# Kernel tuning notes

Hardware: AMD Instinct MI355X
Metric: run time of the kernel (lower is better)

Reference implementation:

```python
import jax, jax.numpy as jnp
import numpy as np

EPS = 1e-5

def _bn(x, gamma, beta):
    # BatchNorm1d training-mode math: batch mean / biased variance over edge dim
    mean = jnp.mean(x, axis=0)
    var = jnp.mean(jnp.square(x - mean), axis=0)
    return (x - mean) * (gamma / jnp.sqrt(var + EPS)) + beta


def setup_inputs() -> dict:
    key = jax.random.key(0)
    ks = jax.random.split(key, 12)
    n, d, s, h, e = 50000, 256, 32, 128, 500000
    feat = 3 * d + s + 1  # 801
    sc = lambda fan_in: 1.0 / np.sqrt(fan_in)
    return {
        "node_embeddings": jax.random.normal(ks[0], (n, d), jnp.float32),
        "gradient_scores": jax.random.normal(ks[1], (e,), jnp.float32),
        "step_embedding": jax.random.normal(ks[2], (s,), jnp.float32),
        "W1": jax.random.normal(ks[3], (feat, h), jnp.float32) * sc(feat),
        "b1": jnp.zeros((h,), jnp.float32),
        "g1": jnp.ones((h,), jnp.float32),
        "be1": jnp.zeros((h,), jnp.float32),
        "W2": jax.random.normal(ks[4], (h, h // 2), jnp.float32) * sc(h),
        "b2": jnp.zeros((h // 2,), jnp.float32),
        "g2": jnp.ones((h // 2,), jnp.float32),
        "be2": jnp.zeros((h // 2,), jnp.float32),
        "W3": jax.random.normal(ks[5], (h // 2, 1), jnp.float32) * sc(h // 2),
        "b3": jnp.zeros((1,), jnp.float32),
        "edge_index": jax.random.randint(ks[6], (2, e), 0, n, jnp.int64),
    }


def reference(node_embeddings, gradient_scores, step_embedding,
              W1, b1, g1, be1, W2, b2, g2, be2, W3, b3, edge_index):
    src, dst = edge_index[0], edge_index[1]
    h_u = node_embeddings[src]              # [E, d]
    h_v = node_embeddings[dst]              # [E, d]
    edge_diff = jnp.abs(h_u - h_v)          # [E, d]
    E = edge_index.shape[1]
    step = jnp.broadcast_to(step_embedding[None, :], (E, step_embedding.shape[0]))
    feats = jnp.concatenate([h_u, h_v, edge_diff, step, gradient_scores[:, None]], axis=1)
    x = jnp.maximum(feats @ W1 + b1, 0.0)
    x = _bn(x, g1, be1)                     # dropout is identity in eval
    x = jnp.maximum(x @ W2 + b2, 0.0)
    x = _bn(x, g2, be2)
    out = jnp.tanh(x @ W3 + b3)[:, 0]       # [E]
    return out
```

## Files before the change

kernel.cpp:

```cpp
#include <hip/hip_runtime.h>

#define NE 500000
#define DIMK 256
#define H1 128
#define H2 64
#define EPSBN 1e-5f
#define GRID1 512
#define NT1 1954
#define GRID2 512
#define NJOBS2 NT1

typedef _Float16 half8 __attribute__((ext_vector_type(8)));
typedef float f32x4 __attribute__((ext_vector_type(4)));
typedef unsigned short ushort8 __attribute__((ext_vector_type(8)));

typedef const __attribute__((address_space(1))) void* gas1_t;
typedef __attribute__((address_space(3))) void* las3_t;

static __device__ __forceinline__ half8 habs8(half8 x) {
  ushort8 u = __builtin_bit_cast(ushort8, x);
  u &= (unsigned short)0x7FFF;
  return __builtin_bit_cast(half8, u);
}
static __device__ __forceinline__ float h2f(unsigned int u) {
  return (float)__builtin_bit_cast(_Float16, (unsigned short)(u & 0xffff));
}
static __device__ __forceinline__ unsigned packf16(float a, float b) {
  unsigned lo = (unsigned)__builtin_bit_cast(unsigned short, (_Float16)a);
  unsigned hi = (unsigned)__builtin_bit_cast(unsigned short, (_Float16)b);
  return lo | (hi << 16);
}
static __device__ __forceinline__ void gload_lds16(const _Float16* src, _Float16* dst) {
  __builtin_amdgcn_global_load_lds((gas1_t)src, (las3_t)dst, 16, 0, 0);
}

#define SB0 __builtin_amdgcn_sched_barrier(0)

__global__ void k_preall(const float* __restrict__ emb, _Float16* __restrict__ embh,
                         const float* __restrict__ W1, _Float16* __restrict__ bfrag,
                         const float* __restrict__ b1, const float* __restrict__ step,
                         float* __restrict__ c0) {
  const int bid = blockIdx.x, t = threadIdx.x;
  if (bid < 6250) {
    const int i = (bid * 256 + t) * 8;
    const float4 a = *(const float4*)(emb + i);
    const float4 b = *(const float4*)(emb + i + 4);
    half8 h;
    h[0] = (_Float16)a.x; h[1] = (_Float16)a.y; h[2] = (_Float16)a.z; h[3] = (_Float16)a.w;
    h[4] = (_Float16)b.x; h[5] = (_Float16)b.y; h[6] = (_Float16)b.z; h[7] = (_Float16)b.w;
    *(half8*)(embh + i) = h;
  } else if (bid < 6298) {
    const int g = (bid - 6250) * 256 + t;
    const int lane = g & 63, f = g >> 6;
    const int c = f & 7, kc = (f >> 3) & 7, s = f >> 6;
    const int row0 = s * 256 + kc * 32 + (lane >> 4) * 8;
    const int col = c * 16 + (lane & 15);
    half8 h;
#pragma unroll
    for (int j = 0; j < 8; ++j) h[j] = (_Float16)W1[(row0 + j) * H1 + col];
    *(half8*)(bfrag + (size_t)g * 8) = h;
  } else {
    if (t < H1) {
      float a = b1[t];
#pragma unroll
      for (int tt = 0; tt < 32; ++tt) a += step[tt] * W1[(768 + tt) * H1 + t];
      c0[t] = a;
    }
  }
}

#define STAGE1(q, kcv) do {                                                   \
    _Pragma("unroll")                                                         \
    for (int jj = 0; jj < 6; ++jj) {                                          \
      const int sc = jj * 4 + w;                                              \
      const int ff = (sc >> 3) * 64 + (kcv) * 8 + (sc & 7);                   \
      gload_lds16(bfrag + ((size_t)ff * 64 + lane) * 8,                       \
                  s_B + (size_t)(q) * 12288 + sc * 512);                      \
    }                                                                         \
  } while (0)

__global__ __launch_bounds__(256, 2)
void k_layer1(const _Float16* __restrict__ embh, const void* __restrict__ eidx_raw,
              const float* __restrict__ grad, const float* __restrict__ W1,
              const float* __restrict__ c0, const _Float16* __restrict__ bfrag,
              _Float16* __restrict__ x1, float* __restrict__ p1) {
  __shared__ int s_src[256], s_dst[256];
  __shared__ float s_g[256];
  __shared__ float s_wg[128], s_c0[128], s_sum[128], s_sq[128];
  __shared__ __align__(16) _Float16 s_B[2 * 12288];

  const int t = threadIdx.x, bid = blockIdx.x;
  const int w = t >> 6, lane = t & 63, quad = lane >> 4, m15 = lane & 15;

  if (t < 128) {
    s_wg[t] = W1[800 * H1 + t];
    s_c0[t] = c0[t];
    s_sum[t] = 0.f; s_sq[t] = 0.f;
  }

  const unsigned* ew = (const unsigned*)eidx_raw;
  const bool is64 = ((ew[1] | ew[3] | ew[5] | ew[7]) == 0u);
  const int* e32 = (const int*)eidx_raw;
  const long long* e64 = (const long long*)eidx_raw;

  float st_s[8] = {0, 0, 0, 0, 0, 0, 0, 0}, st_q[8] = {0, 0, 0, 0, 0, 0, 0, 0};

  for (int tile = bid; tile < NT1; tile += GRID1) {
    const int base = tile * 256;
    __syncthreads();
    {
      int e = base + t; if (e >= NE) e = NE - 1;
      if (is64) { s_src[t] = (int)e64[e]; s_dst[t] = (int)e64[NE + e]; }
      else      { s_src[t] = e32[e];      s_dst[t] = e32[NE + e]; }
      s_g[t] = grad[e];
    }
    STAGE1(0, 0);
    __syncthreads();

    const int r0 = w * 64 + m15;
    const _Float16* pu[4];
    const _Float16* pv[4];
#pragma unroll
    for (int r = 0; r < 4; ++r) {
      pu[r] = embh + (size_t)s_src[r0 + r * 16] * DIMK + quad * 8;
      pv[r] = embh + (size_t)s_dst[r0 + r * 16] * DIMK + quad * 8;
    }
    f32x4 acc[4][8];
#pragma unroll
    for (int r = 0; r < 4; ++r)
#pragma unroll
      for (int c = 0; c < 8; ++c) acc[r][c] = (f32x4)0.f;

#pragma unroll 1
    for (int kc = 0; kc < 8; ++kc) {
      half8 u[4], v[4];
#pragma unroll
      for (int r = 0; r < 4; ++r) {
        u[r] = *(const half8*)(pu[r] + kc * 32);
        v[r] = *(const half8*)(pv[r] + kc * 32);
      }
      SB0;
      asm volatile("s_waitcnt vmcnt(8)" ::: "memory");
      __builtin_amdgcn_s_barrier();
      SB0;
      if (kc < 7) STAGE1((kc + 1) & 1, kc + 1);
      SB0;
      half8 d[4];
#pragma unroll
      for (int r = 0; r < 4; ++r) d[r] = habs8(u[r] - v[r]);

      const half8* bq = (const half8*)s_B + (size_t)(kc & 1) * 1536 + lane;
#pragma unroll
      for (int c = 0; c < 8; ++c) {
        const half8 bu = bq[c * 64];
        const half8 bv = bq[512 + c * 64];
        const half8 bd = bq[1024 + c * 64];
#pragma unroll
        for (int r = 0; r < 4; ++r)
          acc[r][c] = __builtin_amdgcn_mfma_f32_16x16x32_f16(u[r], bu, acc[r][c], 0, 0, 0);
#pragma unroll
        for (int r = 0; r < 4; ++r)
          acc[r][c] = __builtin_amdgcn_mfma_f32_16x16x32_f16(v[r], bv, acc[r][c], 0, 0, 0);
#pragma unroll
        for (int r = 0; r < 4; ++r)
          acc[r][c] = __builtin_amdgcn_mfma_f32_16x16x32_f16(d[r], bd, acc[r][c], 0, 0, 0);
      }
      SB0;
    }
#pragma unroll
    for (int r = 0; r < 4; ++r) {
      const int erow = w * 64 + r * 16 + quad * 4;
#pragma unroll
      for (int c = 0; c < 8; ++c) {
        const int colL = c * 16 + m15;
        const float wgv = s_wg[colL], c0v = s_c0[colL];
#pragma unroll
        for (int reg = 0; reg < 4; ++reg) {
          const int e = base + erow + reg;
          float x = acc[r][c][reg] + s_g[erow + reg] * wgv + c0v;
          x = fmaxf(x, 0.f);
          if (e >= NE) x = 0.f;
          st_s[c] += x; st_q[c] += x * x;
          if (e < NE) x1[(size_t)e * H1 + colL] = (_Float16)x;
        }
      }
    }
  }
  __syncthreads();
#pragma unroll
  for (int c = 0; c < 8; ++c) {
    float a = st_s[c]; a += __shfl_xor(a, 16); a += __shfl_xor(a, 32);
    float b = st_q[c]; b += __shfl_xor(b, 16); b += __shfl_xor(b, 32);
    if (lane < 16) { atomicAdd(&s_sum[c * 16 + m15], a); atomicAdd(&s_sq[c * 16 + m15], b); }
  }
  __syncthreads();
  if (t < 128) {
    p1[t * GRID1 + bid] = s_sum[t];
    p1[128 * GRID1 + t * GRID1 + bid] = s_sq[t];
  }
}

__global__ void k_fin1(const float* __restrict__ p1, const float* __restrict__ g1,
                       const float* __restrict__ be1, const float* __restrict__ W2,
                       const float* __restrict__ b2, float* __restrict__ w2f,
                       float* __restrict__ b2f) {
  __shared__ float s1[128], t1[128];
  const int t = threadIdx.x;
  if (t < 128) {
    float s = 0.f, q = 0.f;
    const float4* rs = (const float4*)(p1 + t * GRID1);
    const float4* rq = (const float4*)(p1 + 128 * GRID1 + t * GRID1);
#pragma unroll 4
    for (int i = 0; i < GRID1 / 4; ++i) {
      float4 a = rs[i]; s += a.x + a.y + a.z + a.w;
      float4 b = rq[i]; q += b.x + b.y + b.z + b.w;
    }
    const float inv = 1.0f / (float)NE;
    float mean = s * inv;
    float var = q * inv - mean * mean;
    float sc = g1[t] * rsqrtf(var + EPSBN);
    s1[t] = sc; t1[t] = be1[t] - mean * sc;
  }
  __syncthreads();
  for (int i = t; i < H1 * H2; i += 256) w2f[i] = s1[i >> 6] * W2[i];
  if (t < 64) {
    float b = b2[t];
    for (int j = 0; j < 128; ++j) b += t1[j] * W2[j * 64 + t];
    b2f[t] = b;
  }
}

__global__ __launch_bounds__(256, 2)
void k_layer2(const _Float16* __restrict__ x1, const float* __restrict__ w2f,
              const float* __restrict__ b2f, _Float16* __restrict__ x2,
              float* __restrict__ p2) {
  __shared__ __align__(16) _Float16 b_lds[8192];
  __shared__ float s_b[64], s_sum[64], s_sq[64];
  const int t = threadIdx.x, bid = blockIdx.x;
  const int w = t >> 6, lane = t & 63, quad = lane >> 4, m15 = lane & 15;

  for (int i = t; i < 8192; i += 256) {
    const int j = i & 7, li = (i >> 3) & 63, f = i >> 9;
    const int c = f & 3, kk = f >> 2;
    const int row = kk * 32 + (li >> 4) * 8 + j;
    const int col = c * 16 + (li & 15);
    b_lds[i] = (_Float16)w2f[row * H2 + col];
  }
  if (t < 64) { s_b[t] = b2f[t]; s_sum[t] = 0.f; s_sq[t] = 0.f; }
  __syncthreads();

  float st_s[4] = {0, 0, 0, 0}, st_q[4] = {0, 0, 0, 0};
  const half8* bp = (const half8*)b_lds;

  for (int job = bid; job < NJOBS2; job += GRID2) {
    const int base = job * 256;
    const _Float16* pa[4];
#pragma unroll
    for (int r = 0; r < 4; ++r) {
      int e = base + w * 64 + r * 16 + m15; if (e >= NE) e = NE - 1;
      pa[r] = x1 + (size_t)e * H1 + quad * 8;
    }
    f32x4 acc[4][4];
#pragma unroll
    for (int r = 0; r < 4; ++r)
#pragma unroll
      for (int c = 0; c < 4; ++c) acc[r][c] = (f32x4)0.f;

#pragma unroll
    for (int kk = 0; kk < 4; ++kk) {
      half8 a[4];
#pragma unroll
      for (int r = 0; r < 4; ++r) a[r] = *(const half8*)(pa[r] + kk * 32);
#pragma unroll
      for (int c = 0; c < 4; ++c) {
        const half8 bf = bp[(kk * 4 + c) * 64 + lane];
#pragma unroll
        for (int r = 0; r < 4; ++r)
          acc[r][c] = __builtin_amdgcn_mfma_f32_16x16x32_f16(a[r], bf, acc[r][c], 0, 0, 0);
      }
    }
#pragma unroll
    for (int r = 0; r < 4; ++r) {
      const int e0 = base + w * 64 + r * 16 + quad * 4;
#pragma unroll
      for (int c = 0; c < 4; ++c) {
        const int colL = c * 16 + m15;
        const float bv = s_b[colL];
        float xv[4];
#pragma unroll
        for (int reg = 0; reg < 4; ++reg) {
          float x = acc[r][c][reg] + bv;
          x = fmaxf(x, 0.f);
          if (e0 + reg >= NE) x = 0.f;
          xv[reg] = x;
          st_s[c] += x; st_q[c] += x * x;
        }
        unsigned b01 = packf16(xv[0], xv[1]);
        unsigned b23 = packf16(xv[2], xv[3]);
        unsigned q01 = (unsigned)__shfl_xor((int)b01, 1);
        unsigned q23 = (unsigned)__shfl_xor((int)b23, 1);
        const int ce = colL & ~1;
        if (!(m15 & 1)) {
          if (e0 < NE)     *(unsigned*)(x2 + (size_t)e0 * H2 + ce)       = (b01 & 0xffffu) | (q01 << 16);
          if (e0 + 1 < NE) *(unsigned*)(x2 + (size_t)(e0 + 1) * H2 + ce) = (b01 >> 16) | (q01 & 0xffff0000u);
        } else {
          if (e0 + 2 < NE) *(unsigned*)(x2 + (size_t)(e0 + 2) * H2 + ce) = (q23 & 0xffffu) | (b23 << 16);
          if (e0 + 3 < NE) *(unsigned*)(x2 + (size_t)(e0 + 3) * H2 + ce) = (q23 >> 16) | (b23 & 0xffff0000u);
        }
      }
    }
  }
  __syncthreads();
#pragma unroll
  for (int c = 0; c < 4; ++c) {
    float a = st_s[c]; a += __shfl_xor(a, 16); a += __shfl_xor(a, 32);
    float b = st_q[c]; b += __shfl_xor(b, 16); b += __shfl_xor(b, 32);
    if (lane < 16) { atomicAdd(&s_sum[c * 16 + m15], a); atomicAdd(&s_sq[c * 16 + m15], b); }
  }
  __syncthreads();
  if (t < 64) {
    p2[t * 512 + bid] = s_sum[t];
    p2[64 * 512 + t * 512 + bid] = s_sq[t];
  }
}

__global__ void k_fin2(const float* __restrict__ p2, const float* __restrict__ g2,
                       const float* __restrict__ be2, const float* __restrict__ W3,
                       const float* __restrict__ b3, float* __restrict__ w3f,
                       float* __restrict__ b3f) {
  __shared__ float tp[64];
  const int t = threadIdx.x;
  if (t < 64) {
    float s = 0.f, q = 0.f;
    const float4* rs = (const float4*)(p2 + t * 512);
    const float4* rq = (const float4*)(p2 + 64 * 512 + t * 512);
#pragma unroll 4
    for (int i = 0; i < 128; ++i) {
      float4 a = rs[i]; s += a.x + a.y + a.z + a.w;
      float4 b = rq[i]; q += b.x + b.y + b.z + b.w;
    }
    const float inv = 1.0f / (float)NE;
    float mean = s * inv;
    float var = q * inv - mean * mean;
    float sc = g2[t] * rsqrtf(var + EPSBN);
    float tt = be2[t] - mean * sc;
    w3f[t] = sc * W3[t];
    tp[t] = tt * W3[t];
  }
  __syncthreads();
  if (t == 0) {
    float b = b3[0];
    for (int j = 0; j < 64; ++j) b += tp[j];
    b3f[0] = b;
  }
}

__global__ __launch_bounds__(256)
void k_out(const unsigned short* __restrict__ x2, const float* __restrict__ w3f,
           const float* __restrict__ b3f, float* __restrict__ out) {
  __shared__ float s_w[64];
  __shared__ float s_b;
  const int t = threadIdx.x;
  if (t < 64) s_w[t] = w3f[t];
  if (t == 0) s_b = b3f[0];
  __syncthreads();
  const int gid = blockIdx.x * 256 + t;
  const int e = gid >> 2, p = gid & 3;
  if (e < NE) {
    const uint4* r = (const uint4*)(x2 + (size_t)e * H2 + p * 16);
    float s = 0.f;
#pragma unroll
    for (int i = 0; i < 2; ++i) {
      const uint4 u = r[i];
      const int jb = p * 16 + i * 8;
      s += h2f(u.x) * s_w[jb + 0] + h2f(u.x >> 16) * s_w[jb + 1];
      s += h2f(u.y) * s_w[jb + 2] + h2f(u.y >> 16) * s_w[jb + 3];
      s += h2f(u.z) * s_w[jb + 4] + h2f(u.z >> 16) * s_w[jb + 5];
      s += h2f(u.w) * s_w[jb + 6] + h2f(u.w >> 16) * s_w[jb + 7];
    }
    s += __shfl_xor(s, 1);
    s += __shfl_xor(s, 2);
    if (p == 0) out[e] = tanhf(s + s_b);
  }
}

extern "C" void kernel_launch(void* const* d_in, const int* in_sizes, int n_in,
                              void* d_out, int out_size, void* d_ws, size_t ws_size,
                              hipStream_t stream) {
  const float* emb  = (const float*)d_in[0];
  const float* grad = (const float*)d_in[1];
  const float* step = (const float*)d_in[2];
  const float* W1   = (const float*)d_in[3];
  const float* b1   = (const float*)d_in[4];
  const float* g1   = (const float*)d_in[5];
  const float* be1  = (const float*)d_in[6];
  const float* W2   = (const float*)d_in[7];
  const float* b2   = (const float*)d_in[8];
  const float* g2   = (const float*)d_in[9];
  const float* be2  = (const float*)d_in[10];
  const float* W3   = (const float*)d_in[11];
  const float* b3   = (const float*)d_in[12];
  const void*  eidx = (const void*)d_in[13];
  float* out = (float*)d_out;

  char* ws = (char*)d_ws;
  _Float16* embh  = (_Float16*)(ws + 0);
  _Float16* x2    = (_Float16*)(ws + 0);
  _Float16* bfrag = (_Float16*)(ws + 25600000LL);
  float*    c0    = (float*)(ws + 25796608LL);
  float*    p1    = (float*)(ws + 26000000LL);
  _Float16* x1    = (_Float16*)(ws + 64000000LL);
  float* p2  = (float*)(ws + 192000000LL);
  float* w2f = (float*)(ws + 192524288LL);
  float* b2f = (float*)(ws + 192557056LL);
  float* w3f = (float*)(ws + 192557312LL);
  float* b3f = (float*)(ws + 192557568LL);

  k_preall<<<6299, 256, 0, stream>>>(emb, embh, W1, bfrag, b1, step, c0);
  k_layer1<<<GRID1,256, 0, stream>>>(embh, eidx, grad, W1, c0, bfrag, x1, p1);
  k_fin1  <<<1,    256, 0, stream>>>(p1, g1, be1, W2, b2, w2f, b2f);
  k_layer2<<<GRID2,256, 0, stream>>>(x1, w2f, b2f, x2, p2);
  k_fin2  <<<1,    128, 0, stream>>>(p2, g2, be2, W3, b3, w3f, b3f);
  k_out   <<<7813, 256, 0, stream>>>((const unsigned short*)x2, w3f, b3f, out);
}
```

Before: 348.3 us.

## Stage gathered edge rows into LDS and use 512-thread layer1 blocks

Layer 1 now runs 512 threads per block (8 waves), with each wave owning 32 edges instead of 64. The gathered node-embedding fragments are loaded with async global_load_lds into a double-buffered LDS tile, prefetched one k-chunk ahead, rather than read into registers. The aim is to overlap the random gather with MFMA work and to cut per-wave register pressure, which should raise occupancy. The cost is more LDS use (an extra 64KB A buffer) and half as many blocks, so each block strides over more tiles.

Result: slower. 362.4 us (+4.1%).

```diff
diff --git a/kernel.cpp b/kernel.cpp
--- a/kernel.cpp
+++ b/kernel.cpp
@@ -5,7 +5,7 @@
 #define H1 128
 #define H2 64
 #define EPSBN 1e-5f
-#define GRID1 512
+#define GRIDL1 256
 #define NT1 1954
 #define GRID2 512
 #define NJOBS2 NT1
@@ -35,6 +35,8 @@
 }
 
 #define SB0 __builtin_amdgcn_sched_barrier(0)
+#define MF(a, b, c) __builtin_amdgcn_mfma_f32_16x16x32_f16(a, b, c, 0, 0, 0)
+#define WAITV(N) asm volatile("s_waitcnt vmcnt(" #N ")" ::: "memory")
 
 __global__ void k_preall(const float* __restrict__ emb, _Float16* __restrict__ embh,
                          const float* __restrict__ W1, _Float16* __restrict__ bfrag,
@@ -69,17 +71,23 @@
   }
 }
 
-#define STAGE1(q, kcv) do {                                                   \
+#define STB(q, kcv) do {                                                      \
     _Pragma("unroll")                                                         \
-    for (int jj = 0; jj < 6; ++jj) {                                          \
-      const int sc = jj * 4 + w;                                              \
+    for (int jj = 0; jj < 3; ++jj) {                                          \
+      const int sc = jj * 8 + w;                                              \
       const int ff = (sc >> 3) * 64 + (kcv) * 8 + (sc & 7);                   \
       gload_lds16(bfrag + ((size_t)ff * 64 + lane) * 8,                       \
                   s_B + (size_t)(q) * 12288 + sc * 512);                      \
     }                                                                         \
   } while (0)
 
-__global__ __launch_bounds__(256, 2)
+#define STA(q, kcv) do {                                                      \
+    _Pragma("unroll")                                                         \
+    for (int fi = 0; fi < 4; ++fi)                                            \
+      gload_lds16(pA[fi] + (kcv) * 32, &s_A[q][w][fi][0]);                    \
+  } while (0)
+
+__global__ __launch_bounds__(512, 2)
 void k_layer1(const _Float16* __restrict__ embh, const void* __restrict__ eidx_raw,
               const float* __restrict__ grad, const float* __restrict__ W1,
               const float* __restrict__ c0, const _Float16* __restrict__ bfrag,
@@ -88,6 +96,7 @@
   __shared__ float s_g[256];
   __shared__ float s_wg[128], s_c0[128], s_sum[128], s_sq[128];
   __shared__ __align__(16) _Float16 s_B[2 * 12288];
+  __shared__ __align__(16) _Float16 s_A[2][8][4][512];
 
   const int t = threadIdx.x, bid = blockIdx.x;
   const int w = t >> 6, lane = t & 63, quad = lane >> 4, m15 = lane & 15;
@@ -105,78 +114,73 @@
 
   float st_s[8] = {0, 0, 0, 0, 0, 0, 0, 0}, st_q[8] = {0, 0, 0, 0, 0, 0, 0, 0};
 
-  for (int tile = bid; tile < NT1; tile += GRID1) {
+  for (int tile = bid; tile < NT1; tile += GRIDL1) {
     const int base = tile * 256;
     __syncthreads();
-    {
+    if (t < 256) {
       int e = base + t; if (e >= NE) e = NE - 1;
       if (is64) { s_src[t] = (int)e64[e]; s_dst[t] = (int)e64[NE + e]; }
       else      { s_src[t] = e32[e];      s_dst[t] = e32[NE + e]; }
       s_g[t] = grad[e];
     }
-    STAGE1(0, 0);
     __syncthreads();
 
-    const int r0 = w * 64 + m15;
-    const _Float16* pu[4];
-    const _Float16* pv[4];
-#pragma unroll
-    for (int r = 0; r < 4; ++r) {
-      pu[r] = embh + (size_t)s_src[r0 + r * 16] * DIMK + quad * 8;
-      pv[r] = embh + (size_t)s_dst[r0 + r * 16] * DIMK + quad * 8;
-    }
-    f32x4 acc[4][8];
-#pragma unroll
-    for (int r = 0; r < 4; ++r)
+    const _Float16* pA[4];
+#pragma unroll
+    for (int fi = 0; fi < 4; ++fi) {
+      const int* idx = (fi < 2) ? s_src : s_dst;
+      const int e = idx[w * 32 + (fi & 1) * 16 + m15];
+      pA[fi] = embh + (size_t)e * DIMK + quad * 8;
+    }
+    SB0;
+    STB(0, 0);
+    STA(0, 0);
+    SB0;
+
+    f32x4 acc[2][8];
+#pragma unroll
+    for (int r = 0; r < 2; ++r)
 #pragma unroll
       for (int c = 0; c < 8; ++c) acc[r][c] = (f32x4)0.f;
 
 #pragma unroll 1
     for (int kc = 0; kc < 8; ++kc) {
-      half8 u[4], v[4];
-#pragma unroll
-      for (int r = 0; r < 4; ++r) {
-        u[r] = *(const half8*)(pu[r] + kc * 32);
-        v[r] = *(const half8*)(pv[r] + kc * 32);
-      }
+      if (kc < 7) { STA((kc + 1) & 1, kc + 1); SB0; WAITV(4); }
+      else        { SB0; WAITV(0); }
       SB0;
-      asm volatile("s_waitcnt vmcnt(8)" ::: "memory");
       __builtin_amdgcn_s_barrier();
       SB0;
-      if (kc < 7) STAGE1((kc + 1) & 1, kc + 1);
+      if (kc < 7) STB((kc + 1) & 1, kc + 1);
       SB0;
-      half8 d[4];
-#pragma unroll
-      for (int r = 0; r < 4; ++r) d[r] = habs8(u[r] - v[r]);
-
+      const _Float16* ab = &s_A[kc & 1][w][0][0];
+      const half8 u0 = *(const half8*)(ab + (size_t)lane * 8);
+      const half8 u1 = *(const half8*)(ab + 512 + (size_t)lane * 8);
+      const half8 v0 = *(const half8*)(ab + 1024 + (size_t)lane * 8);
+      const half8 v1 = *(const half8*)(ab + 1536 + (size_t)lane * 8);
+      const half8 d0 = habs8(u0 - v0), d1 = habs8(u1 - v1);
       const half8* bq = (const half8*)s_B + (size_t)(kc & 1) * 1536 + lane;
 #pragma unroll
       for (int c = 0; c < 8; ++c) {
         const half8 bu = bq[c * 64];
         const half8 bv = bq[512 + c * 64];
         const half8 bd = bq[1024 + c * 64];
-#pragma unroll
-        for (int r = 0; r < 4; ++r)
-          acc[r][c] = __builtin_amdgcn_mfma_f32_16x16x32_f16(u[r], bu, acc[r][c], 0, 0, 0);
-#pragma unroll
-        for (int r = 0; r < 4; ++r)
-          acc[r][c] = __builtin_amdgcn_mfma_f32_16x16x32_f16(v[r], bv, acc[r][c], 0, 0, 0);
-#pragma unroll
-        for (int r = 0; r < 4; ++r)
-          acc[r][c] = __builtin_amdgcn_mfma_f32_16x16x32_f16(d[r], bd, acc[r][c], 0, 0, 0);
+        acc[0][c] = MF(u0, bu, acc[0][c]); acc[1][c] = MF(u1, bu, acc[1][c]);
+        acc[0][c] = MF(v0, bv, acc[0][c]); acc[1][c] = MF(v1, bv, acc[1][c]);
+        acc[0][c] = MF(d0, bd, acc[0][c]); acc[1][c] = MF(d1, bd, acc[1][c]);
       }
       SB0;
     }
 #pragma unroll
-    for (int r = 0; r < 4; ++r) {
-      const int erow = w * 64 + r * 16 + quad * 4;
+    for (int r = 0; r < 2; ++r) {
+      const int erow = w * 32 + r * 16 + quad * 4;
+      const int e0 = base + erow;
 #pragma unroll
       for (int c = 0; c < 8; ++c) {
         const int colL = c * 16 + m15;
         const float wgv = s_wg[colL], c0v = s_c0[colL];
 #pragma unroll
         for (int reg = 0; reg < 4; ++reg) {
-          const int e = base + erow + reg;
+          const int e = e0 + reg;
           float x = acc[r][c][reg] + s_g[erow + reg] * wgv + c0v;
           x = fmaxf(x, 0.f);
           if (e >= NE) x = 0.f;
@@ -195,8 +199,8 @@
   }
   __syncthreads();
   if (t < 128) {
-    p1[t * GRID1 + bid] = s_sum[t];
-    p1[128 * GRID1 + t * GRID1 + bid] = s_sq[t];
+    p1[t * GRIDL1 + bid] = s_sum[t];
+    p1[128 * GRIDL1 + t * GRIDL1 + bid] = s_sq[t];
   }
 }
 
@@ -208,10 +212,10 @@
   const int t = threadIdx.x;
   if (t < 128) {
     float s = 0.f, q = 0.f;
-    const float4* rs = (const float4*)(p1 + t * GRID1);
-    const float4* rq = (const float4*)(p1 + 128 * GRID1 + t * GRID1);
+    const float4* rs = (const float4*)(p1 + t * GRIDL1);
+    const float4* rq = (const float4*)(p1 + 128 * GRIDL1 + t * GRIDL1);
 #pragma unroll 4
-    for (int i = 0; i < GRID1 / 4; ++i) {
+    for (int i = 0; i < GRIDL1 / 4; ++i) {
       float4 a = rs[i]; s += a.x + a.y + a.z + a.w;
       float4 b = rq[i]; q += b.x + b.y + b.z + b.w;
     }
@@ -416,10 +420,10 @@
   float* w3f = (float*)(ws + 192557312LL);
   float* b3f = (float*)(ws + 192557568LL);
 
-  k_preall<<<6299, 256, 0, stream>>>(emb, embh, W1, bfrag, b1, step, c0);
-  k_layer1<<<GRID1,256, 0, stream>>>(embh, eidx, grad, W1, c0, bfrag, x1, p1);
-  k_fin1  <<<1,    256, 0, stream>>>(p1, g1, be1, W2, b2, w2f, b2f);
-  k_layer2<<<GRID2,256, 0, stream>>>(x1, w2f, b2f, x2, p2);
-  k_fin2  <<<1,    128, 0, stream>>>(p2, g2, be2, W3, b3, w3f, b3f);
-  k_out   <<<7813, 256, 0, stream>>>((const unsigned short*)x2, w3f, b3f, out);
-}
+  k_preall<<<6299,  256, 0, stream>>>(emb, embh, W1, bfrag, b1, step, c0);
+  k_layer1<<<GRIDL1,512, 0, stream>>>(embh, eidx, grad, W1, c0, bfrag, x1, p1);
+  k_fin1  <<<1,     256, 0, stream>>>(p1, g1, be1, W2, b2, w2f, b2f);
+  k_layer2<<<GRID2, 256, 0, stream>>>(x1, w2f, b2f, x2, p2);
+  k_fin2  <<<1,     128, 0, stream>>>(p2, g2, be2, W3, b3, w3f, b3f);
+  k_out   <<<7813,  256, 0, stream>>>((const unsigned short*)x2, w3f, b3f, out);
+}
```
